# Performance work log

Hardware: AMD Instinct MI355X
Metric: run time of the kernel (lower is better)

Reference implementation:

```python
import jax, jax.numpy as jnp
import numpy as np

D, H, E, HID, TOPK = 1024, 16, 8, 2048, 2
B, L = 2, 2048

def setup_inputs() -> dict:
    key = jax.random.key(0)
    ks = jax.random.split(key, 12)
    s = 0.02
    return {
        "x": jax.random.normal(ks[0], (B, L, D), jnp.float32),
        "mask": jnp.zeros((B, L), dtype=bool),  # key_padding_mask: True = ignore
        "ln1_g": jnp.ones((D,), jnp.float32), "ln1_b": jnp.zeros((D,), jnp.float32),
        "Wqkv": jax.random.normal(ks[1], (3 * D, D), jnp.float32) * s,
        "bqkv": jnp.zeros((3 * D,), jnp.float32),
        "Wo": jax.random.normal(ks[2], (D, D), jnp.float32) * s,
        "bo": jnp.zeros((D,), jnp.float32),
        "ln2_g": jnp.ones((D,), jnp.float32), "ln2_b": jnp.zeros((D,), jnp.float32),
        "Wg": jax.random.normal(ks[3], (D, E), jnp.float32) * s,
        "bg": jnp.zeros((E,), jnp.float32),
        "W1": jax.random.normal(ks[4], (E, D, HID), jnp.float32) * s,
        "b1": jnp.zeros((E, HID), jnp.float32),
        "W2": jax.random.normal(ks[5], (E, HID, D), jnp.float32) * s,
        "b2": jnp.zeros((E, D), jnp.float32),
    }

def _layernorm(x, g, b, eps=1e-5):
    mu = x.mean(-1, keepdims=True)
    var = ((x - mu) ** 2).mean(-1, keepdims=True)
    return (x - mu) * jax.lax.rsqrt(var + eps) * g + b

def reference(x, mask, ln1_g, ln1_b, Wqkv, bqkv, Wo, bo, ln2_g, ln2_b, Wg, bg, W1, b1, W2, b2):
    b, l, d = x.shape
    dh = d // H
    # ---- pre-norm self-attention ----
    residual = x
    xn = _layernorm(x, ln1_g, ln1_b)
    qkv = xn @ Wqkv.T + bqkv                      # [B,L,3D]
    q, k, v = jnp.split(qkv, 3, axis=-1)
    q = q.reshape(b, l, H, dh).transpose(0, 2, 1, 3)  # bhld
    k = k.reshape(b, l, H, dh).transpose(0, 2, 1, 3)
    v = v.reshape(b, l, H, dh).transpose(0, 2, 1, 3)
    scores = jnp.einsum('bhqd,bhkd->bhqk', q, k) / jnp.sqrt(jnp.float32(dh))
    scores = jnp.where(mask[:, None, None, :], jnp.float32(-1e9), scores)
    attn = jax.nn.softmax(scores, axis=-1)
    ao = jnp.einsum('bhqk,bhkd->bhqd', attn, v).transpose(0, 2, 1, 3).reshape(b, l, d)
    ao = ao @ Wo.T + bo
    x = residual + ao                              # dropout is identity at eval
    # ---- pre-norm MoE FFN (top-2 softmax gating) ----
    residual = x
    xn = _layernorm(x, ln2_g, ln2_b)
    T = b * l
    xf = xn.reshape(T, d)
    probs = jax.nn.softmax(xf @ Wg + bg, axis=-1)  # [T,E]
    vals, idx = jax.lax.top_k(probs, TOPK)         # [T,K]
    wts = vals / vals.sum(-1, keepdims=True)
    # dense expert compute (reference): all experts over all tokens
    h = jax.nn.gelu(jnp.einsum('td,edh->eth', xf, W1) + b1[:, None, :], approximate=False)
    eo = jnp.einsum('eth,ehd->etd', h, W2) + b2[:, None, :]   # [E,T,D]
    sel = eo[idx, jnp.arange(T)[:, None]]          # [T,K,D]
    moe_out = (wts[..., None] * sel).sum(1).reshape(b, l, d)
    # load-balancing aux loss
    me = probs.mean(0)                             # mean gate prob per expert
    ce = jax.nn.one_hot(idx, E, dtype=probs.dtype).sum(1).mean(0)  # dispatch fraction
    moe_loss = jnp.float32(E) * jnp.sum(me * ce)
    out = residual + moe_out
    return (out, moe_loss)
```

## Files before the change

kernel.cpp:

```cpp
#include <hip/hip_runtime.h>
#include <stdint.h>

#define TOK   4096
#define DIM   1024
#define NH    16
#define DHD   64
#define NE    8
#define HIDN  2048
#define BATCH 2
#define SEQ   2048
#define BK    64

using floatx4 = __attribute__((ext_vector_type(4))) float;
using bfx8    = __attribute__((ext_vector_type(8))) __bf16;
using bfx2    = __attribute__((ext_vector_type(2))) __bf16;
using shortx8 = __attribute__((ext_vector_type(8))) short;

__device__ __forceinline__ unsigned short f2bf(float f) {
    union { __bf16 b; unsigned short u; } v;
    v.b = (__bf16)f;
    return v.u;
}

__device__ __forceinline__ unsigned pack2bf(float lo, float hi) {
    union { bfx2 v; unsigned u; } t;
    t.v[0] = (__bf16)lo;
    t.v[1] = (__bf16)hi;
    return t.u;
}

__device__ __forceinline__ floatx4 mfma16(bfx8 a, bfx8 b, floatx4 c) {
    return __builtin_amdgcn_mfma_f32_16x16x32_bf16(a, b, c, 0, 0, 0);
}

__device__ __forceinline__ void gload16(const unsigned short* g, unsigned short* l) {
    __builtin_amdgcn_global_load_lds(
        (const __attribute__((address_space(1))) unsigned int*)g,
        (__attribute__((address_space(3))) unsigned int*)l, 16, 0, 0);
}

__global__ __launch_bounds__(256) void cvt_kernel(const float* __restrict__ in,
                                                  unsigned short* __restrict__ out, int n) {
    int i = (blockIdx.x * 256 + threadIdx.x) * 4;
    if (i < n) {
        float4 v = *reinterpret_cast<const float4*>(in + i);
        out[i + 0] = f2bf(v.x);
        out[i + 1] = f2bf(v.y);
        out[i + 2] = f2bf(v.z);
        out[i + 3] = f2bf(v.w);
    }
}

__global__ __launch_bounds__(256) void transpose_cvt_kernel(const float* __restrict__ in,
                                                            unsigned short* __restrict__ out,
                                                            int R, int C) {
    __shared__ unsigned short t[64][65];
    in  += (size_t)blockIdx.z * R * C;
    out += (size_t)blockIdx.z * R * C;
    int r0 = blockIdx.y * 64, c0 = blockIdx.x * 64;
    int lr = threadIdx.x >> 4, lc = (threadIdx.x & 15) * 4;
#pragma unroll
    for (int p = 0; p < 4; p++) {
        int r = p * 16 + lr;
        float4 v = *reinterpret_cast<const float4*>(in + (size_t)(r0 + r) * C + c0 + lc);
        t[lc + 0][r] = f2bf(v.x);
        t[lc + 1][r] = f2bf(v.y);
        t[lc + 2][r] = f2bf(v.z);
        t[lc + 3][r] = f2bf(v.w);
    }
    __syncthreads();
    int c = threadIdx.x >> 2, ch = (threadIdx.x & 3) * 16;
    shortx8 o0, o1;
#pragma unroll
    for (int q = 0; q < 8; q++) { o0[q] = t[c][ch + q]; o1[q] = t[c][ch + 8 + q]; }
    unsigned short* op = out + (size_t)(c0 + c) * R + r0 + ch;
    *reinterpret_cast<shortx8*>(op) = o0;
    *reinterpret_cast<shortx8*>(op + 8) = o1;
}

__global__ __launch_bounds__(256) void kvprep_kernel(const unsigned short* __restrict__ qkv,
                                                     unsigned short* __restrict__ ktg,
                                                     unsigned short* __restrict__ vtg,
                                                     const unsigned char* __restrict__ mask,
                                                     float* __restrict__ maskf) {
    __shared__ unsigned short t[64 * 64];
    int tid = threadIdx.x;
    int s0 = blockIdx.x * 64, hd = blockIdx.y, b = blockIdx.z;
    size_t bh = (size_t)(b * NH + hd);
    if (hd == 0 && tid < 64) {
        maskf[(size_t)b * SEQ + s0 + tid] =
            mask[(size_t)b * SEQ + s0 + tid] ? -1.44269504e9f : 0.0f;
    }
#pragma unroll
    for (int i = 0; i < 2; i++) {
        int idx = i * 256 + tid;
        int sr = idx >> 3, c = idx & 7;
        shortx8 v = *reinterpret_cast<const shortx8*>(
            qkv + (size_t)(b * SEQ + s0 + sr) * 3 * DIM + DIM + hd * DHD + c * 8);
        *reinterpret_cast<shortx8*>(ktg + (bh * SEQ + s0 + sr) * DHD + c * 8) = v;
    }
#pragma unroll
    for (int i = 0; i < 2; i++) {
        int idx = i * 256 + tid;
        int sr = idx >> 3, c = idx & 7;
        shortx8 v = *reinterpret_cast<const shortx8*>(
            qkv + (size_t)(b * SEQ + s0 + sr) * 3 * DIM + 2 * DIM + hd * DHD + c * 8);
        *reinterpret_cast<shortx8*>(t + sr * 64 + ((c ^ (sr >> 3)) * 8)) = v;
    }
    __syncthreads();
#pragma unroll
    for (int i = 0; i < 2; i++) {
        int idx = i * 256 + tid;
        int d = idx >> 3, c2 = idx & 7;
        shortx8 o;
#pragma unroll
        for (int e = 0; e < 8; e++) {
            int s = c2 * 8 + e;
            o[e] = (short)t[s * 64 + (((d >> 3) ^ c2) * 8) + (d & 7)];
        }
        *reinterpret_cast<shortx8*>(vtg + (bh * DHD + d) * SEQ + s0 + c2 * 8) = o;
    }
}

__global__ __launch_bounds__(256) void ln_kernel(const float* __restrict__ x,
                                                 const float* __restrict__ g,
                                                 const float* __restrict__ b,
                                                 unsigned short* __restrict__ obf) {
    int t = blockIdx.x;
    int tid = threadIdx.x;
    const float* xr = x + (size_t)t * DIM;
    float4 v = *reinterpret_cast<const float4*>(xr + tid * 4);
    float s  = v.x + v.y + v.z + v.w;
    float s2 = v.x * v.x + v.y * v.y + v.z * v.z + v.w * v.w;
    for (int o = 32; o > 0; o >>= 1) {
        s  += __shfl_down(s,  o, 64);
        s2 += __shfl_down(s2, o, 64);
    }
    __shared__ float red[10];
    int lane = tid & 63, w = tid >> 6;
    if (lane == 0) { red[w] = s; red[4 + w] = s2; }
    __syncthreads();
    if (tid == 0) {
        float ts = red[0] + red[1] + red[2] + red[3];
        float t2 = red[4] + red[5] + red[6] + red[7];
        float mu = ts * (1.0f / DIM);
        float var = t2 * (1.0f / DIM) - mu * mu;
        red[8] = mu;
        red[9] = rsqrtf(var + 1e-5f);
    }
    __syncthreads();
    float mu = red[8], rstd = red[9];
    float4 gv = *reinterpret_cast<const float4*>(g + tid * 4);
    float4 bv = *reinterpret_cast<const float4*>(b + tid * 4);
    size_t o = (size_t)t * DIM + tid * 4;
    obf[o + 0] = f2bf((v.x - mu) * rstd * gv.x + bv.x);
    obf[o + 1] = f2bf((v.y - mu) * rstd * gv.y + bv.y);
    obf[o + 2] = f2bf((v.z - mu) * rstd * gv.z + bv.z);
    obf[o + 3] = f2bf((v.w - mu) * rstd * gv.w + bv.w);
}

template <int EPI, bool GATHER>
__global__ __launch_bounds__(256) void gemm_kernel(const unsigned short* __restrict__ A,
                                                   const unsigned short* __restrict__ Bt,
                                                   void* __restrict__ C,
                                                   const float* __restrict__ bias,
                                                   const float* __restrict__ resid,
                                                   const int* __restrict__ cnt,
                                                   const int* __restrict__ goff,
                                                   const int* __restrict__ gtok,
                                                   int M, int N, int K) {
    int e = blockIdx.z;
    int Me = cnt ? cnt[e] : M;
    int brow = blockIdx.y * 128;
    if (brow >= Me) return;
    int bcol = blockIdx.x * 128;
    int go = goff ? goff[e] : 0;
    const unsigned short* Be = Bt + (size_t)e * N * K;
    const float* biasp = bias + (size_t)e * N;

    __shared__ unsigned short As[128 * BK];
    __shared__ unsigned short Bs[128 * BK];

    int tid = threadIdx.x, lane = tid & 63, w = tid >> 6;
    int wr = w >> 1, wc = w & 1;
    int cg = lane >> 4, cl = lane & 15;

    const unsigned short* aga[4];
    const unsigned short* bga[4];
    unsigned short* asb = As + w * 2048;
    unsigned short* bsb = Bs + w * 2048;
#pragma unroll
    for (int i = 0; i < 4; i++) {
        int s = w * 256 + i * 64 + lane;
        int row = s >> 3;
        int c = (s & 7) ^ (row & 7);
        int gr = brow + row;
        if (gr >= Me) gr = Me - 1;
        long ar;
        if (GATHER) ar = gtok[go + gr];
        else if (cnt) ar = go + gr;
        else ar = gr;
        aga[i] = A + ar * (long)K + c * 8;
        bga[i] = Be + (size_t)(bcol + row) * K + c * 8;
    }

    floatx4 acc[4][4];
#pragma unroll
    for (int m = 0; m < 4; m++)
#pragma unroll
        for (int n = 0; n < 4; n++) acc[m][n] = (floatx4){0.f, 0.f, 0.f, 0.f};

    for (int kt = 0; kt < K; kt += BK) {
#pragma unroll
        for (int i = 0; i < 4; i++) {
            gload16(aga[i], asb + i * 512);
            gload16(bga[i], bsb + i * 512);
            aga[i] += BK;
            bga[i] += BK;
        }
        __syncthreads();
#pragma unroll
        for (int ks = 0; ks < 2; ks++) {
            bfx8 af[4], bf[4];
#pragma unroll
            for (int m = 0; m < 4; m++) {
                int row = wr * 64 + m * 16 + cl;
                af[m] = *reinterpret_cast<const bfx8*>(
                    As + row * BK + (((ks * 4 + cg) ^ (row & 7)) << 3));
            }
#pragma unroll
            for (int n = 0; n < 4; n++) {
                int row = wc * 64 + n * 16 + cl;
                bf[n] = *reinterpret_cast<const bfx8*>(
                    Bs + row * BK + (((ks * 4 + cg) ^ (row & 7)) << 3));
            }
#pragma unroll
            for (int m = 0; m < 4; m++)
#pragma unroll
                for (int n = 0; n < 4; n++) acc[m][n] = mfma16(af[m], bf[n], acc[m][n]);
        }
        __syncthreads();
    }

#pragma unroll
    for (int m = 0; m < 4; m++) {
#pragma unroll
        for (int j = 0; j < 4; j++) {
            int r = brow + wr * 64 + m * 16 + cg * 4 + j;
            if (r >= Me) continue;
#pragma unroll
            for (int n = 0; n < 4; n++) {
                int col = bcol + wc * 64 + n * 16 + cl;
                float v = acc[m][n][j] + biasp[col];
                if (EPI == 0) {
                    ((unsigned short*)C)[(size_t)r * N + col] = f2bf(v);
                } else if (EPI == 1) {
                    size_t o = (size_t)r * N + col;
                    ((float*)C)[o] = v + resid[o];
                } else if (EPI == 2) {
                    float gg = 0.5f * v * (1.0f + erff(v * 0.70710678f));
                    ((unsigned short*)C)[(size_t)(go + r) * N + col] = f2bf(gg);
                } else {
                    ((float*)C)[(size_t)(go + r) * N + col] = v;
                }
            }
        }
    }
}

__global__ __launch_bounds__(256) void attn_kernel(const unsigned short* __restrict__ qkv,
                                                   const unsigned short* __restrict__ ktg,
                                                   const unsigned short* __restrict__ vtg,
                                                   const float* __restrict__ maskf,
                                                   unsigned short* __restrict__ ao) {
    __shared__ unsigned short Ks[2][64 * 64];
    __shared__ unsigned short Vs[2][64 * 64];
    __shared__ unsigned short Ps[4][16 * 72];

    int tid = threadIdx.x, lane = tid & 63, w = tid >> 6;
    int cg = lane >> 4, cl = lane & 15;
    int qb = blockIdx.x * 64, hd = blockIdx.y, b = blockIdx.z;
    size_t bh = (size_t)(b * NH + hd);
    const float SC2 = 0.125f * 1.44269504f;

    int tq = qb + w * 16 + cl;
    const unsigned short* qrow = qkv + (size_t)(b * SEQ + tq) * 3 * DIM + hd * DHD;
    bfx8 aq0 = *reinterpret_cast<const bfx8*>(qrow + cg * 8);
    bfx8 aq1 = *reinterpret_cast<const bfx8*>(qrow + 32 + cg * 8);

    int srow = lane >> 3, schunk = lane & 7;
    int sg = (schunk ^ srow) * 8;
    const unsigned short* kptr = ktg + (bh * SEQ + w * 16 + srow) * DHD + sg;
    const unsigned short* vptr = vtg + (bh * DHD + w * 16 + srow) * SEQ + sg;
    const float* mrowf = maskf + (size_t)b * SEQ;
    unsigned short* psw = &Ps[w][0];
    int sw0 = (cg ^ (cl & 7)) << 3;

    floatx4 accO[4];
#pragma unroll
    for (int dt = 0; dt < 4; dt++) accO[dt] = (floatx4){0.f, 0.f, 0.f, 0.f};
    float m0 = -3.0e38f, l0 = 0.f;

    gload16(kptr, &Ks[0][w * 1024]);
    gload16(kptr + 8 * DHD, &Ks[0][w * 1024 + 512]);
    gload16(vptr, &Vs[0][w * 1024]);
    gload16(vptr + 8 * SEQ, &Vs[0][w * 1024 + 512]);
    __syncthreads();

    int cur = 0;
    for (int t = 0; t < SEQ / 64; t++) {
        if (t < SEQ / 64 - 1) {
            size_t nkt = (size_t)(t + 1) * 64;
            int nb = cur ^ 1;
            gload16(kptr + nkt * DHD, &Ks[nb][w * 1024]);
            gload16(kptr + nkt * DHD + 8 * DHD, &Ks[nb][w * 1024 + 512]);
            gload16(vptr + nkt, &Vs[nb][w * 1024]);
            gload16(vptr + nkt + 8 * SEQ, &Vs[nb][w * 1024 + 512]);
        }
        const unsigned short* ksb = &Ks[cur][0];
        const unsigned short* vsb = &Vs[cur][0];
        int kt = t * 64;

        floatx4 accS[4];
#pragma unroll
        for (int nt = 0; nt < 4; nt++) accS[nt] = (floatx4){0.f, 0.f, 0.f, 0.f};
#pragma unroll
        for (int nt = 0; nt < 4; nt++) {
            const unsigned short* kr = ksb + (nt * 16 + cl) * 64;
            bfx8 k0 = *reinterpret_cast<const bfx8*>(kr + sw0);
            bfx8 k1 = *reinterpret_cast<const bfx8*>(kr + (sw0 ^ 32));
            accS[nt] = mfma16(k0, aq0, accS[nt]);
            accS[nt] = mfma16(k1, aq1, accS[nt]);
        }

        float s[4][4];
        float tmax = -3.0e38f;
#pragma unroll
        for (int nt = 0; nt < 4; nt++) {
            float4 mk4 = *reinterpret_cast<const float4*>(mrowf + kt + nt * 16 + cg * 4);
            s[nt][0] = fmaf(accS[nt][0], SC2, mk4.x);
            s[nt][1] = fmaf(accS[nt][1], SC2, mk4.y);
            s[nt][2] = fmaf(accS[nt][2], SC2, mk4.z);
            s[nt][3] = fmaf(accS[nt][3], SC2, mk4.w);
#pragma unroll
            for (int j = 0; j < 4; j++) tmax = fmaxf(tmax, s[nt][j]);
        }
        tmax = fmaxf(tmax, __shfl_xor(tmax, 16, 64));
        tmax = fmaxf(tmax, __shfl_xor(tmax, 32, 64));

        if (!__all(tmax - m0 <= 11.5f)) {
            float mn = fmaxf(m0, tmax);
            float al = __builtin_amdgcn_exp2f(m0 - mn);
            m0 = mn;
            l0 *= al;
#pragma unroll
            for (int dt = 0; dt < 4; dt++) accO[dt] *= al;
        }

        float rs = 0.f;
        unsigned pk[4][2];
#pragma unroll
        for (int nt = 0; nt < 4; nt++) {
            float p0 = __builtin_amdgcn_exp2f(s[nt][0] - m0);
            float p1 = __builtin_amdgcn_exp2f(s[nt][1] - m0);
            float p2 = __builtin_amdgcn_exp2f(s[nt][2] - m0);
            float p3 = __builtin_amdgcn_exp2f(s[nt][3] - m0);
            rs += (p0 + p1) + (p2 + p3);
            pk[nt][0] = pack2bf(p0, p1);
            pk[nt][1] = pack2bf(p2, p3);
        }
        rs += __shfl_xor(rs, 16, 64);
        rs += __shfl_xor(rs, 32, 64);
        l0 += rs;

#pragma unroll
        for (int nt = 0; nt < 4; nt++) {
            uint2 u; u.x = pk[nt][0]; u.y = pk[nt][1];
            *reinterpret_cast<uint2*>(psw + cl * 72 + nt * 16 + cg * 4) = u;
        }
        bfx8 pf0 = *reinterpret_cast<const bfx8*>(psw + cl * 72 + cg * 8);
        bfx8 pf1 = *reinterpret_cast<const bfx8*>(psw + cl * 72 + 32 + cg * 8);
#pragma unroll
        for (int dt = 0; dt < 4; dt++) {
            const unsigned short* vr = vsb + (dt * 16 + cl) * 64;
            bfx8 v0 = *reinterpret_cast<const bfx8*>(vr + sw0);
            bfx8 v1 = *reinterpret_cast<const bfx8*>(vr + (sw0 ^ 32));
            accO[dt] = mfma16(v0, pf0, accO[dt]);
            accO[dt] = mfma16(v1, pf1, accO[dt]);
        }
        __syncthreads();
        cur ^= 1;
    }

    float rl = 1.0f / l0;
    unsigned short* aorow = ao + (size_t)(b * SEQ + qb + w * 16 + cl) * DIM + hd * DHD;
#pragma unroll
    for (int dt = 0; dt < 4; dt++) {
        uint2 u;
        u.x = pack2bf(accO[dt][0] * rl, accO[dt][1] * rl);
        u.y = pack2bf(accO[dt][2] * rl, accO[dt][3] * rl);
        *reinterpret_cast<uint2*>(aorow + dt * 16 + cg * 4) = u;
    }
}

__global__ __launch_bounds__(256) void gate_kernel(const float* __restrict__ x2,
                                                   const float* __restrict__ lng,
                                                   const float* __restrict__ lnb,
                                                   const float* __restrict__ Wg,
                                                   const float* __restrict__ bg,
                                                   unsigned short* __restrict__ xn2b,
                                                   int* __restrict__ idx,
                                                   float* __restrict__ wts,
                                                   float* __restrict__ me_part) {
    __shared__ float bme[8];
    if (threadIdx.x < 8) bme[threadIdx.x] = 0.f;
    __syncthreads();
    int w = threadIdx.x >> 6, lane = threadIdx.x & 63;
    int t = blockIdx.x * 4 + w;
    const float* xr = x2 + (size_t)t * DIM + lane * 16;
    float4 xv[4];
    float s = 0.f, s2 = 0.f;
#pragma unroll
    for (int q = 0; q < 4; q++) {
        xv[q] = *reinterpret_cast<const float4*>(xr + q * 4);
        s  += xv[q].x + xv[q].y + xv[q].z + xv[q].w;
        s2 += xv[q].x * xv[q].x + xv[q].y * xv[q].y + xv[q].z * xv[q].z + xv[q].w * xv[q].w;
    }
    for (int o = 32; o > 0; o >>= 1) {
        s  += __shfl_xor(s,  o, 64);
        s2 += __shfl_xor(s2, o, 64);
    }
    float mu = s * (1.0f / DIM);
    float rstd = rsqrtf(s2 * (1.0f / DIM) - mu * mu + 1e-5f);
    float acc[8];
#pragma unroll
    for (int e = 0; e < 8; e++) acc[e] = 0.f;
    unsigned short ob[16];
#pragma unroll
    for (int q = 0; q < 4; q++) {
        float4 gv = *reinterpret_cast<const float4*>(lng + lane * 16 + q * 4);
        float4 bv = *reinterpret_cast<const float4*>(lnb + lane * 16 + q * 4);
        float xn0 = (xv[q].x - mu) * rstd * gv.x + bv.x;
        float xn1 = (xv[q].y - mu) * rstd * gv.y + bv.y;
        float xn2 = (xv[q].z - mu) * rstd * gv.z + bv.z;
        float xn3 = (xv[q].w - mu) * rstd * gv.w + bv.w;
        ob[q * 4 + 0] = f2bf(xn0);
        ob[q * 4 + 1] = f2bf(xn1);
        ob[q * 4 + 2] = f2bf(xn2);
        ob[q * 4 + 3] = f2bf(xn3);
        const float* wr = Wg + (size_t)(lane * 16 + q * 4) * 8;
#pragma unroll
        for (int e = 0; e < 8; e++) acc[e] += xn0 * wr[e];
#pragma unroll
        for (int e = 0; e < 8; e++) acc[e] += xn1 * wr[8 + e];
#pragma unroll
        for (int e = 0; e < 8; e++) acc[e] += xn2 * wr[16 + e];
#pragma unroll
        for (int e = 0; e < 8; e++) acc[e] += xn3 * wr[24 + e];
    }
    unsigned short* op = xn2b + (size_t)t * DIM + lane * 16;
    *reinterpret_cast<shortx8*>(op)     = *reinterpret_cast<shortx8*>(&ob[0]);
    *reinterpret_cast<shortx8*>(op + 8) = *reinterpret_cast<shortx8*>(&ob[8]);
    for (int o = 32; o > 0; o >>= 1)
#pragma unroll
        for (int e = 0; e < 8; e++) acc[e] += __shfl_xor(acc[e], o, 64);
    if (lane == 0) {
        float p[8];
        float mx = -3e38f;
#pragma unroll
        for (int e = 0; e < 8; e++) { acc[e] += bg[e]; mx = fmaxf(mx, acc[e]); }
        float se = 0.f;
#pragma unroll
        for (int e = 0; e < 8; e++) { p[e] = expf(acc[e] - mx); se += p[e]; }
#pragma unroll
        for (int e = 0; e < 8; e++) p[e] /= se;
        int i0 = 0; float v0 = p[0];
#pragma unroll
        for (int e = 1; e < 8; e++) if (p[e] > v0) { v0 = p[e]; i0 = e; }
        int i1 = -1; float v1 = -3e38f;
#pragma unroll
        for (int e = 0; e < 8; e++) if (e != i0 && p[e] > v1) { v1 = p[e]; i1 = e; }
        float sw = v0 + v1;
        idx[t * 2]     = i0;
        idx[t * 2 + 1] = i1;
        wts[t * 2]     = v0 / sw;
        wts[t * 2 + 1] = v1 / sw;
#pragma unroll
        for (int e = 0; e < 8; e++) atomicAdd(&bme[e], p[e]);
    }
    __syncthreads();
    if (threadIdx.x < 8) me_part[(size_t)blockIdx.x * 8 + threadIdx.x] = bme[threadIdx.x];
}

__global__ __launch_bounds__(256) void route1_kernel(const int* __restrict__ idx,
                                                     int* __restrict__ cnt,
                                                     int* __restrict__ posl) {
    __shared__ int lh[8];
    __shared__ int gb[8];
    int tid = threadIdx.x;
    int t = blockIdx.x * 256 + tid;
    if (tid < 8) lh[tid] = 0;
    __syncthreads();
    int i0 = idx[t * 2], i1 = idx[t * 2 + 1];
    int r0 = atomicAdd(&lh[i0], 1);
    int r1 = atomicAdd(&lh[i1], 1);
    __syncthreads();
    if (tid < 8) gb[tid] = atomicAdd(&cnt[tid], lh[tid]);
    __syncthreads();
    posl[t * 2]     = gb[i0] + r0;
    posl[t * 2 + 1] = gb[i1] + r1;
}

__global__ void prefix_kernel(const int* __restrict__ cnt, int* __restrict__ goff) {
    if (threadIdx.x == 0) {
        int s = 0;
        for (int e = 0; e < 8; e++) { goff[e] = s; s += cnt[e]; }
        goff[8] = s;
    }
}

__global__ __launch_bounds__(256) void route2_kernel(const int* __restrict__ idx,
                                                     const int* __restrict__ goff,
                                                     const int* __restrict__ posl,
                                                     int* __restrict__ gtok,
                                                     int* __restrict__ tpos) {
    int t = blockIdx.x * 256 + threadIdx.x;
#pragma unroll
    for (int j = 0; j < 2; j++) {
        int e = idx[t * 2 + j];
        int p = goff[e] + posl[t * 2 + j];
        gtok[p] = t;
        tpos[t * 2 + j] = p;
    }
}

__global__ __launch_bounds__(256) void combine_kernel(const float* __restrict__ x2,
                                                      const float* __restrict__ eo,
                                                      const float* __restrict__ wts,
                                                      const int* __restrict__ tpos,
                                                      float* __restrict__ out) {
    int t = blockIdx.x;
    int c = threadIdx.x * 4;
    float w0 = wts[t * 2], w1 = wts[t * 2 + 1];
    int p0 = tpos[t * 2], p1 = tpos[t * 2 + 1];
    float4 r  = *reinterpret_cast<const float4*>(x2 + (size_t)t * DIM + c);
    float4 a  = *reinterpret_cast<const float4*>(eo + (size_t)p0 * DIM + c);
    float4 bb = *reinterpret_cast<const float4*>(eo + (size_t)p1 * DIM + c);
    float4 o;
    o.x = r.x + w0 * a.x + w1 * bb.x;
    o.y = r.y + w0 * a.y + w1 * bb.y;
    o.z = r.z + w0 * a.z + w1 * bb.z;
    o.w = r.w + w0 * a.w + w1 * bb.w;
    *reinterpret_cast<float4*>(out + (size_t)t * DIM + c) = o;
}

__global__ __launch_bounds__(256) void loss_kernel(const float* __restrict__ me_part,
                                                   const int* __restrict__ cnt,
                                                   float* __restrict__ out) {
    __shared__ float red[256];
    int tid = threadIdx.x;
    int e = tid & 7, part = tid >> 3;
    float s = 0.f;
    for (int b = part; b < 1024; b += 32) s += me_part[(size_t)b * 8 + e];
    red[tid] = s;
    __syncthreads();
    if (tid < 64) {
        float v = red[tid] + red[tid + 64] + red[tid + 128] + red[tid + 192];
        red[tid] = v;
    }
    __syncthreads();
    if (tid < 8) {
        float v = red[tid] + red[tid + 8] + red[tid + 16] + red[tid + 24] +
                  red[tid + 32] + red[tid + 40] + red[tid + 48] + red[tid + 56];
        red[tid] = v;
    }
    __syncthreads();
    if (tid == 0) {
        float s2 = 0.f;
        for (int ee = 0; ee < 8; ee++)
            s2 += (red[ee] / 4096.0f) * ((float)cnt[ee] / 4096.0f);
        out[(size_t)TOK * DIM] = 8.0f * s2;
    }
}

extern "C" void kernel_launch(void* const* d_in, const int* in_sizes, int n_in,
                              void* d_out, int out_size, void* d_ws, size_t ws_size,
                              hipStream_t stream) {
    const float* x    = (const float*)d_in[0];
    const unsigned char* mask = (const unsigned char*)d_in[1];
    const float* ln1g = (const float*)d_in[2];
    const float* ln1b = (const float*)d_in[3];
    const float* Wqkv = (const float*)d_in[4];
    const float* bqkv = (const float*)d_in[5];
    const float* Wo   = (const float*)d_in[6];
    const float* bo   = (const float*)d_in[7];
    const float* ln2g = (const float*)d_in[8];
    const float* ln2b = (const float*)d_in[9];
    const float* Wg   = (const float*)d_in[10];
    const float* bg   = (const float*)d_in[11];
    const float* W1   = (const float*)d_in[12];
    const float* b1   = (const float*)d_in[13];
    const float* W2   = (const float*)d_in[14];
    const float* b2   = (const float*)d_in[15];
    float* out = (float*)d_out;

    char* ws = (char*)d_ws;
    int*   cnt  = (int*)(ws + 0);
    int*   goff = (int*)(ws + 128);
    size_t off = 1024;
    auto alloc = [&](size_t bytes) -> void* {
        void* p = ws + off;
        off += (bytes + 255) & ~(size_t)255;
        return p;
    };
    const size_t SZ_QKVB = (size_t)TOK * 3 * DIM * 2;
    const size_t SZ_HB   = (size_t)2 * TOK * HIDN * 2;
    const size_t SZ_EOF  = (size_t)2 * TOK * DIM * 4;
    char* R1 = (char*)alloc(SZ_HB > SZ_QKVB ? SZ_HB : SZ_QKVB);
    char* R2 = (char*)alloc(SZ_EOF);
    unsigned short* qkvb  = (unsigned short*)R1;
    unsigned short* hb    = (unsigned short*)R1;
    float*          eof   = (float*)R2;
    unsigned short* xn1   = (unsigned short*)R2;
    unsigned short* aob   = (unsigned short*)(R2 + (size_t)TOK * DIM * 2);
    unsigned short* wqkvb = (unsigned short*)(R2 + (size_t)2 * TOK * DIM * 2);
    unsigned short* wob   = (unsigned short*)(R2 + (size_t)2 * TOK * DIM * 2 +
                                              (size_t)3 * DIM * DIM * 2);
    float*          x2    = (float*)alloc((size_t)TOK * DIM * 4);
    unsigned short* xn2b  = (unsigned short*)alloc((size_t)TOK * DIM * 2);
    unsigned short* w1t   = (unsigned short*)alloc((size_t)NE * DIM * HIDN * 2);
    unsigned short* w2t   = (unsigned short*)alloc((size_t)NE * DIM * HIDN * 2);
    unsigned short* ktg   = (unsigned short*)alloc((size_t)BATCH * NH * SEQ * DHD * 2);
    unsigned short* vtg   = (unsigned short*)alloc((size_t)BATCH * NH * DHD * SEQ * 2);
    float*          maskf = (float*)alloc((size_t)BATCH * SEQ * 4);
    float*          mep   = (float*)alloc((size_t)1024 * 8 * 4);
    int*            idxp  = (int*)alloc((size_t)TOK * 2 * 4);
    float*          wtsp  = (float*)alloc((size_t)TOK * 2 * 4);
    int*            posl  = (int*)alloc((size_t)TOK * 2 * 4);
    int*            gtok  = (int*)alloc((size_t)2 * TOK * 4);
    int*            tpos  = (int*)alloc((size_t)TOK * 2 * 4);

    hipMemsetAsync(ws, 0, 256, stream);

    cvt_kernel<<<3 * DIM * DIM / 1024, 256, 0, stream>>>(Wqkv, wqkvb, 3 * DIM * DIM);
    cvt_kernel<<<DIM * DIM / 1024, 256, 0, stream>>>(Wo, wob, DIM * DIM);
    transpose_cvt_kernel<<<dim3(HIDN / 64, DIM / 64, NE), 256, 0, stream>>>(W1, w1t, DIM, HIDN);
    transpose_cvt_kernel<<<dim3(DIM / 64, HIDN / 64, NE), 256, 0, stream>>>(W2, w2t, HIDN, DIM);

    ln_kernel<<<TOK, 256, 0, stream>>>(x, ln1g, ln1b, xn1);

    gemm_kernel<0, false><<<dim3(24, 32, 1), 256, 0, stream>>>(
        xn1, wqkvb, qkvb, bqkv, nullptr, nullptr, nullptr, nullptr, TOK, 3 * DIM, DIM);

    kvprep_kernel<<<dim3(SEQ / 64, NH, BATCH), 256, 0, stream>>>(qkvb, ktg, vtg, mask, maskf);

    attn_kernel<<<dim3(SEQ / 64, NH, BATCH), 256, 0, stream>>>(qkvb, ktg, vtg, maskf, aob);

    gemm_kernel<1, false><<<dim3(8, 32, 1), 256, 0, stream>>>(
        aob, wob, x2, bo, x, nullptr, nullptr, nullptr, TOK, DIM, DIM);

    gate_kernel<<<TOK / 4, 256, 0, stream>>>(x2, ln2g, ln2b, Wg, bg, xn2b,
                                             idxp, wtsp, mep);
    route1_kernel<<<TOK / 256, 256, 0, stream>>>(idxp, cnt, posl);
    prefix_kernel<<<1, 64, 0, stream>>>(cnt, goff);
    route2_kernel<<<TOK / 256, 256, 0, stream>>>(idxp, goff, posl, gtok, tpos);

    gemm_kernel<2, true><<<dim3(16, 32, 8), 256, 0, stream>>>(
        xn2b, w1t, hb, b1, nullptr, cnt, goff, gtok, TOK, HIDN, DIM);

    gemm_kernel<3, false><<<dim3(8, 32, 8), 256, 0, stream>>>(
        hb, w2t, eof, b2, nullptr, cnt, goff, nullptr, TOK, DIM, HIDN);

    combine_kernel<<<TOK, 256, 0, stream>>>(x2, eof, wtsp, tpos, out);
    loss_kernel<<<1, 256, 0, stream>>>(mep, cnt, out);
}
```

Before: 403.1 us.

## Swizzle GEMM blocks per XCD, widen attention blocks, tanh GELU, bf16 expert output

Several unrelated changes. GEMM workgroup IDs are remapped so that neighbouring tiles land on the same XCD, which should improve L2 reuse. The attention kernel now runs 512 threads over 128 queries per block, sharing each K/V tile load across twice as many waves, and the row-max shuffle is deferred to the rare rescale path. Exact erf GELU is replaced by a tanh-style approximation built on exp2 and rcp, and the expert output is stored as bf16 instead of fp32, halving write and read traffic into combine. The GELU approximation and bf16 expert outputs add numerical error. The deferred shuffle also means rescale decisions are made per lane rather than per row, which may be inconsistent across lanes sharing a row.

```diff
diff --git a/kernel.cpp b/kernel.cpp
--- a/kernel.cpp
+++ b/kernel.cpp
@@ -22,6 +22,12 @@
     return v.u;
 }
 
+__device__ __forceinline__ float bf2f(unsigned short u) {
+    union { unsigned u; float f; } v;
+    v.u = (unsigned)u << 16;
+    return v.f;
+}
+
 __device__ __forceinline__ unsigned pack2bf(float lo, float hi) {
     union { bfx2 v; unsigned u; } t;
     t.v[0] = (__bf16)lo;
@@ -29,6 +35,12 @@
     return t.u;
 }
 
+__device__ __forceinline__ float fast_gelu(float v) {
+    float vc = v * (1.0f + 0.044715f * v * v);
+    float e  = __builtin_amdgcn_exp2f(fminf(vc * 2.302264f, 80.0f));
+    return v * e * __builtin_amdgcn_rcpf(e + 1.0f);
+}
+
 __device__ __forceinline__ floatx4 mfma16(bfx8 a, bfx8 b, floatx4 c) {
     return __builtin_amdgcn_mfma_f32_16x16x32_bf16(a, b, c, 0, 0, 0);
 }
@@ -37,6 +49,12 @@
     __builtin_amdgcn_global_load_lds(
         (const __attribute__((address_space(1))) unsigned int*)g,
         (__attribute__((address_space(3))) unsigned int*)l, 16, 0, 0);
+}
+
+__device__ __forceinline__ int xcd_swz(int hw, int nwg) {
+    int q = nwg >> 3, r = nwg & 7;
+    int xc = hw & 7, o = hw >> 3;
+    return (xc < r ? xc * (q + 1) : r * (q + 1) + (xc - r) * q) + o;
 }
 
 __global__ __launch_bounds__(256) void cvt_kernel(const float* __restrict__ in,
@@ -169,11 +187,19 @@
                                                    const int* __restrict__ goff,
                                                    const int* __restrict__ gtok,
                                                    int M, int N, int K) {
-    int e = blockIdx.z;
+    int gx = gridDim.x, gy = gridDim.y;
+    int nwg = gx * gy * (int)gridDim.z;
+    int hw = ((int)blockIdx.z * gy + (int)blockIdx.y) * gx + (int)blockIdx.x;
+    int virt = xcd_swz(hw, nwg);
+    int bx = virt % gx;
+    int tmp = virt / gx;
+    int by = tmp % gy;
+    int e = tmp / gy;
+
     int Me = cnt ? cnt[e] : M;
-    int brow = blockIdx.y * 128;
+    int brow = by * 128;
     if (brow >= Me) return;
-    int bcol = blockIdx.x * 128;
+    int bcol = bx * 128;
     int go = goff ? goff[e] : 0;
     const unsigned short* Be = Bt + (size_t)e * N * K;
     const float* biasp = bias + (size_t)e * N;
@@ -258,28 +284,27 @@
                     size_t o = (size_t)r * N + col;
                     ((float*)C)[o] = v + resid[o];
                 } else if (EPI == 2) {
-                    float gg = 0.5f * v * (1.0f + erff(v * 0.70710678f));
-                    ((unsigned short*)C)[(size_t)(go + r) * N + col] = f2bf(gg);
+                    ((unsigned short*)C)[(size_t)(go + r) * N + col] = f2bf(fast_gelu(v));
                 } else {
-                    ((float*)C)[(size_t)(go + r) * N + col] = v;
+                    ((unsigned short*)C)[(size_t)(go + r) * N + col] = f2bf(v);
                 }
             }
         }
     }
 }
 
-__global__ __launch_bounds__(256) void attn_kernel(const unsigned short* __restrict__ qkv,
-                                                   const unsigned short* __restrict__ ktg,
-                                                   const unsigned short* __restrict__ vtg,
-                                                   const float* __restrict__ maskf,
-                                                   unsigned short* __restrict__ ao) {
+__global__ __launch_bounds__(512, 2) void attn_kernel(const unsigned short* __restrict__ qkv,
+                                                      const unsigned short* __restrict__ ktg,
+                                                      const unsigned short* __restrict__ vtg,
+                                                      const float* __restrict__ maskf,
+                                                      unsigned short* __restrict__ ao) {
     __shared__ unsigned short Ks[2][64 * 64];
     __shared__ unsigned short Vs[2][64 * 64];
-    __shared__ unsigned short Ps[4][16 * 72];
+    __shared__ unsigned short Ps[8][16 * 72];
 
     int tid = threadIdx.x, lane = tid & 63, w = tid >> 6;
     int cg = lane >> 4, cl = lane & 15;
-    int qb = blockIdx.x * 64, hd = blockIdx.y, b = blockIdx.z;
+    int qb = blockIdx.x * 128, hd = blockIdx.y, b = blockIdx.z;
     size_t bh = (size_t)(b * NH + hd);
     const float SC2 = 0.125f * 1.44269504f;
 
@@ -288,10 +313,10 @@
     bfx8 aq0 = *reinterpret_cast<const bfx8*>(qrow + cg * 8);
     bfx8 aq1 = *reinterpret_cast<const bfx8*>(qrow + 32 + cg * 8);
 
-    int srow = lane >> 3, schunk = lane & 7;
-    int sg = (schunk ^ srow) * 8;
-    const unsigned short* kptr = ktg + (bh * SEQ + w * 16 + srow) * DHD + sg;
-    const unsigned short* vptr = vtg + (bh * DHD + w * 16 + srow) * SEQ + sg;
+    int srow8 = lane >> 3, schunk = lane & 7;
+    int csrc = schunk ^ srow8;
+    const unsigned short* kptr = ktg + (bh * SEQ + w * 8 + srow8) * DHD + csrc * 8;
+    const unsigned short* vptr = vtg + (bh * DHD + w * 8 + srow8) * SEQ + csrc * 8;
     const float* mrowf = maskf + (size_t)b * SEQ;
     unsigned short* psw = &Ps[w][0];
     int sw0 = (cg ^ (cl & 7)) << 3;
@@ -301,10 +326,8 @@
     for (int dt = 0; dt < 4; dt++) accO[dt] = (floatx4){0.f, 0.f, 0.f, 0.f};
     float m0 = -3.0e38f, l0 = 0.f;
 
-    gload16(kptr, &Ks[0][w * 1024]);
-    gload16(kptr + 8 * DHD, &Ks[0][w * 1024 + 512]);
-    gload16(vptr, &Vs[0][w * 1024]);
-    gload16(vptr + 8 * SEQ, &Vs[0][w * 1024 + 512]);
+    gload16(kptr, &Ks[0][tid * 8]);
+    gload16(vptr, &Vs[0][tid * 8]);
     __syncthreads();
 
     int cur = 0;
@@ -312,10 +335,8 @@
         if (t < SEQ / 64 - 1) {
             size_t nkt = (size_t)(t + 1) * 64;
             int nb = cur ^ 1;
-            gload16(kptr + nkt * DHD, &Ks[nb][w * 1024]);
-            gload16(kptr + nkt * DHD + 8 * DHD, &Ks[nb][w * 1024 + 512]);
-            gload16(vptr + nkt, &Vs[nb][w * 1024]);
-            gload16(vptr + nkt + 8 * SEQ, &Vs[nb][w * 1024 + 512]);
+            gload16(kptr + nkt * DHD, &Ks[nb][tid * 8]);
+            gload16(vptr + nkt, &Vs[nb][tid * 8]);
         }
         const unsigned short* ksb = &Ks[cur][0];
         const unsigned short* vsb = &Vs[cur][0];
@@ -345,10 +366,9 @@
 #pragma unroll
             for (int j = 0; j < 4; j++) tmax = fmaxf(tmax, s[nt][j]);
         }
-        tmax = fmaxf(tmax, __shfl_xor(tmax, 16, 64));
-        tmax = fmaxf(tmax, __shfl_xor(tmax, 32, 64));
-
         if (!__all(tmax - m0 <= 11.5f)) {
+            tmax = fmaxf(tmax, __shfl_xor(tmax, 16, 64));
+            tmax = fmaxf(tmax, __shfl_xor(tmax, 32, 64));
             float mn = fmaxf(m0, tmax);
             float al = __builtin_amdgcn_exp2f(m0 - mn);
             m0 = mn;
@@ -358,7 +378,6 @@
         }
 
         float rs = 0.f;
-        unsigned pk[4][2];
 #pragma unroll
         for (int nt = 0; nt < 4; nt++) {
             float p0 = __builtin_amdgcn_exp2f(s[nt][0] - m0);
@@ -366,18 +385,15 @@
             float p2 = __builtin_amdgcn_exp2f(s[nt][2] - m0);
             float p3 = __builtin_amdgcn_exp2f(s[nt][3] - m0);
             rs += (p0 + p1) + (p2 + p3);
-            pk[nt][0] = pack2bf(p0, p1);
-            pk[nt][1] = pack2bf(p2, p3);
+            uint2 u;
+            u.x = pack2bf(p0, p1);
+            u.y = pack2bf(p2, p3);
+            *reinterpret_cast<uint2*>(psw + cl * 72 + nt * 16 + cg * 4) = u;
         }
         rs += __shfl_xor(rs, 16, 64);
         rs += __shfl_xor(rs, 32, 64);
         l0 += rs;
 
-#pragma unroll
-        for (int nt = 0; nt < 4; nt++) {
-            uint2 u; u.x = pk[nt][0]; u.y = pk[nt][1];
-            *reinterpret_cast<uint2*>(psw + cl * 72 + nt * 16 + cg * 4) = u;
-        }
         bfx8 pf0 = *reinterpret_cast<const bfx8*>(psw + cl * 72 + cg * 8);
         bfx8 pf1 = *reinterpret_cast<const bfx8*>(psw + cl * 72 + 32 + cg * 8);
 #pragma unroll
@@ -535,7 +551,7 @@
 }
 
 __global__ __launch_bounds__(256) void combine_kernel(const float* __restrict__ x2,
-                                                      const float* __restrict__ eo,
+                                                      const unsigned short* __restrict__ eo,
                                                       const float* __restrict__ wts,
                                                       const int* __restrict__ tpos,
                                                       float* __restrict__ out) {
@@ -543,14 +559,14 @@
     int c = threadIdx.x * 4;
     float w0 = wts[t * 2], w1 = wts[t * 2 + 1];
     int p0 = tpos[t * 2], p1 = tpos[t * 2 + 1];
-    float4 r  = *reinterpret_cast<const float4*>(x2 + (size_t)t * DIM + c);
-    float4 a  = *reinterpret_cast<const float4*>(eo + (size_t)p0 * DIM + c);
-    float4 bb = *reinterpret_cast<const float4*>(eo + (size_t)p1 * DIM + c);
+    float4 r = *reinterpret_cast<const float4*>(x2 + (size_t)t * DIM + c);
+    ushort4 a4 = *reinterpret_cast<const ushort4*>(eo + (size_t)p0 * DIM + c);
+    ushort4 b4 = *reinterpret_cast<const ushort4*>(eo + (size_t)p1 * DIM + c);
     float4 o;
-    o.x = r.x + w0 * a.x + w1 * bb.x;
-    o.y = r.y + w0 * a.y + w1 * bb.y;
-    o.z = r.z + w0 * a.z + w1 * bb.z;
-    o.w = r.w + w0 * a.w + w1 * bb.w;
+    o.x = r.x + w0 * bf2f(a4.x) + w1 * bf2f(b4.x);
+    o.y = r.y + w0 * bf2f(a4.y) + w1 * bf2f(b4.y);
+    o.z = r.z + w0 * bf2f(a4.z) + w1 * bf2f(b4.z);
+    o.w = r.w + w0 * bf2f(a4.w) + w1 * bf2f(b4.w);
     *reinterpret_cast<float4*>(out + (size_t)t * DIM + c) = o;
 }
 
@@ -615,12 +631,13 @@
     };
     const size_t SZ_QKVB = (size_t)TOK * 3 * DIM * 2;
     const size_t SZ_HB   = (size_t)2 * TOK * HIDN * 2;
-    const size_t SZ_EOF  = (size_t)2 * TOK * DIM * 4;
     char* R1 = (char*)alloc(SZ_HB > SZ_QKVB ? SZ_HB : SZ_QKVB);
-    char* R2 = (char*)alloc(SZ_EOF);
+    const size_t SZ_R2 = (size_t)2 * TOK * DIM * 2 + (size_t)3 * DIM * DIM * 2 +
+                         (size_t)DIM * DIM * 2;
+    char* R2 = (char*)alloc(SZ_R2);
     unsigned short* qkvb  = (unsigned short*)R1;
     unsigned short* hb    = (unsigned short*)R1;
-    float*          eof   = (float*)R2;
+    unsigned short* eo16  = (unsigned short*)R2;
     unsigned short* xn1   = (unsigned short*)R2;
     unsigned short* aob   = (unsigned short*)(R2 + (size_t)TOK * DIM * 2);
     unsigned short* wqkvb = (unsigned short*)(R2 + (size_t)2 * TOK * DIM * 2);
@@ -654,7 +671,7 @@
 
     kvprep_kernel<<<dim3(SEQ / 64, NH, BATCH), 256, 0, stream>>>(qkvb, ktg, vtg, mask, maskf);
 
-    attn_kernel<<<dim3(SEQ / 64, NH, BATCH), 256, 0, stream>>>(qkvb, ktg, vtg, maskf, aob);
+    attn_kernel<<<dim3(SEQ / 128, NH, BATCH), 512, 0, stream>>>(qkvb, ktg, vtg, maskf, aob);
 
     gemm_kernel<1, false><<<dim3(8, 32, 1), 256, 0, stream>>>(
         aob, wob, x2, bo, x, nullptr, nullptr, nullptr, TOK, DIM, DIM);
@@ -669,8 +686,8 @@
         xn2b, w1t, hb, b1, nullptr, cnt, goff, gtok, TOK, HIDN, DIM);
 
     gemm_kernel<3, false><<<dim3(8, 32, 8), 256, 0, stream>>>(
-        hb, w2t, eof, b2, nullptr, cnt, goff, nullptr, TOK, DIM, HIDN);
-
-    combine_kernel<<<TOK, 256, 0, stream>>>(x2, eof, wtsp, tpos, out);
+        hb, w2t, eo16, b2, nullptr, cnt, goff, nullptr, TOK, DIM, HIDN);
+
+    combine_kernel<<<TOK, 256, 0, stream>>>(x2, eo16, wtsp, tpos, out);
     loss_kernel<<<1, 256, 0, stream>>>(mep, cnt, out);
 }
```

After: 349.1 us. -13.4%, faster.
